# Kernel optimization log

Hardware: AMD Instinct MI355X
Metric: run time of the kernel (lower is better)

## Reference

```python
import jax, jax.numpy as jnp
import numpy as np

EPS = 1e-5
DEG = 2  # polynomial degree of each resgconv layer (adj powers 0..DEG-1)


def _bn(x):
    # repo's functional batchnorm(x, axis=1): standardize over the node axis per event
    m = x.mean(axis=1, keepdims=True)
    s = x.std(axis=1, keepdims=True)
    return (x - m) / (s + EPS)


def _adj(phi, eta):
    # Gaussian kernel of squared euclidean distance in the (eta, phi) plane
    d2 = (phi[:, :, None] - phi[:, None, :]) ** 2 + (eta[:, :, None] - eta[:, None, :]) ** 2
    return jnp.exp(-d2)  # [B, N, N]


def _resgconv(adj, x, W, b, Wr, br):
    # x: [B, C_in, N]; spread = concat of adj^k @ x for k in 0..DEG-1 over channels
    sp = [x]
    cur = x
    for _ in range(DEG - 1):
        cur = jnp.einsum('bij,bcj->bci', adj, cur)
        sp.append(cur)
    sp = jnp.concatenate(sp, axis=1)  # [B, C_in*DEG, N]
    out = jnp.einsum('oc,bcn->bon', W, sp) + b[None, :, None]
    res = jnp.einsum('oc,bcn->bon', Wr, x) + br[None, :, None]  # residual shortcut
    return jax.nn.relu(out) + res


def setup_inputs():
    key = jax.random.key(0)
    ks = jax.random.split(key, 32)
    B, N = 16, 2048
    dims = [3, 64, 64, 64, 64]
    inp = {
        'e': jax.random.normal(ks[0], (B, N), dtype=jnp.float32),
        'phi': jax.random.normal(ks[1], (B, N), dtype=jnp.float32),
        'eta': jax.random.normal(ks[2], (B, N), dtype=jnp.float32),
    }
    for i in range(4):
        cin, cout = dims[i], dims[i + 1]
        inp[f'W{i}'] = jax.random.normal(ks[3 + 4 * i], (cout, cin * DEG)) * (1.0 / np.sqrt(cin * DEG))
        inp[f'b{i}'] = jnp.zeros((cout,), dtype=jnp.float32)
        inp[f'Wr{i}'] = jax.random.normal(ks[4 + 4 * i], (cout, cin)) * (1.0 / np.sqrt(cin))
        inp[f'br{i}'] = jnp.zeros((cout,), dtype=jnp.float32)
    inp['fcW'] = jax.random.normal(ks[30], (1, dims[-1])) * (1.0 / np.sqrt(dims[-1]))
    inp['fcb'] = jnp.zeros((1,), dtype=jnp.float32)
    return inp


def reference(e, phi, eta, W0, b0, Wr0, br0, W1, b1, Wr1, br1, W2, b2, Wr2, br2, W3, b3, Wr3, br3, fcW, fcb):
    en = _bn(e)
    adj = _adj(phi, eta)
    x = jnp.stack([en, _bn(eta), _bn(phi)], axis=1)  # [B, 3, N]
    for (W, b, Wr, br) in ((W0, b0, Wr0, br0), (W1, b1, Wr1, br1), (W2, b2, Wr2, br2), (W3, b3, Wr3, br3)):
        x = _resgconv(adj, x, W, b, Wr, br)
    pooled = x.mean(axis=2)  # [B, C]
    out = pooled @ fcW.T + fcb  # [B, 1]
    return out[:, 0]
```

## Files before the change

### kernel.cpp

```cpp
#include <hip/hip_runtime.h>
#include <hip/hip_bf16.h>

#define NN 2048
#define NB 16
#define XT_PITCH 88
#define CAT_PITCH 136
#define RED_PITCH 132

typedef __attribute__((ext_vector_type(8))) short short8;
typedef __attribute__((ext_vector_type(4))) float f32x4;

static __device__ __forceinline__ float bfbits2f(short s) {
  unsigned int u = ((unsigned int)(unsigned short)s) << 16;
  float f; __builtin_memcpy(&f, &u, 4); return f;
}
static __device__ __forceinline__ short f2bfbits(float f) {
  __hip_bfloat16 h = __float2bfloat16(f);
  unsigned short us; __builtin_memcpy(&us, &h, 2); return (short)us;
}
static __device__ __forceinline__ float exp2_fast(float x) {
#if __has_builtin(__builtin_amdgcn_exp2f)
  return __builtin_amdgcn_exp2f(x);
#else
  return exp2f(x);
#endif
}
static __device__ __forceinline__ unsigned pack2bf(float f0, float f1) {
  unsigned u0, u1;
  __builtin_memcpy(&u0, &f0, 4);
  __builtin_memcpy(&u1, &f1, 4);
  return __builtin_amdgcn_perm(u1 + 0x8000u, u0 + 0x8000u, 0x07060302u);
}

__global__ __launch_bounds__(256) void bn_kernel(
    const float* __restrict__ e, const float* __restrict__ phi,
    const float* __restrict__ eta, __hip_bfloat16* __restrict__ x0) {
  const int b = blockIdx.x;
  const int c = blockIdx.y;
  const int t = threadIdx.x;
  __hip_bfloat16* out = x0 + ((size_t)b * 64 + c) * NN;
  if (c >= 3) {
    short8 z = {0, 0, 0, 0, 0, 0, 0, 0};
    for (int idx = t * 8; idx < NN; idx += 256 * 8) *(short8*)&out[idx] = z;
    return;
  }
  const float* src = (c == 0 ? e : (c == 1 ? eta : phi)) + (size_t)b * NN;
  float sum = 0.f, sq = 0.f;
  for (int idx = t * 4; idx < NN; idx += 256 * 4) {
    float4 v = *(const float4*)&src[idx];
    sum += v.x + v.y + v.z + v.w;
    sq += v.x * v.x + v.y * v.y + v.z * v.z + v.w * v.w;
  }
  __shared__ float rs[256], rq[256];
  rs[t] = sum; rq[t] = sq;
  __syncthreads();
  for (int off = 128; off > 0; off >>= 1) {
    if (t < off) { rs[t] += rs[t + off]; rq[t] += rq[t + off]; }
    __syncthreads();
  }
  const float m = rs[0] * (1.f / NN);
  const float var = fmaxf(rq[0] * (1.f / NN) - m * m, 0.f);
  const float rinv = 1.f / (sqrtf(var) + 1e-5f);
  for (int idx = t * 4; idx < NN; idx += 256 * 4) {
    float4 v = *(const float4*)&src[idx];
    out[idx + 0] = __float2bfloat16((v.x - m) * rinv);
    out[idx + 1] = __float2bfloat16((v.y - m) * rinv);
    out[idx + 2] = __float2bfloat16((v.z - m) * rinv);
    out[idx + 3] = __float2bfloat16((v.w - m) * rinv);
  }
}

__global__ __launch_bounds__(256) void prep_kernel(
    const float* __restrict__ W0, const float* __restrict__ W1,
    const float* __restrict__ W2, const float* __restrict__ W3,
    const float* __restrict__ R0, const float* __restrict__ R1,
    const float* __restrict__ R2, const float* __restrict__ R3,
    short* __restrict__ blob) {
  const int layer = blockIdx.x;
  const float* W = layer == 0 ? W0 : layer == 1 ? W1 : layer == 2 ? W2 : W3;
  const float* R = layer == 0 ? R0 : layer == 1 ? R1 : layer == 2 ? R2 : R3;
  const int CIN = layer == 0 ? 3 : 64;
  short* base = blob + layer * 24576;
  for (int f = threadIdx.x; f < 8192; f += 256) {
    int e = f & 7, lane = (f >> 3) & 63, ks = (f >> 9) & 3, os = f >> 11;
    int o = os * 16 + (lane & 15);
    int k = ks * 32 + (lane >> 4) * 8 + e;
    float v = 0.f;
    if (k < 64) { if (k < CIN) v = W[o * 2 * CIN + k]; }
    else { int c = k - 64; if (c < CIN) v = W[o * 2 * CIN + CIN + c]; }
    short hi = f2bfbits(v);
    base[f] = hi;
    base[8192 + f] = f2bfbits(v - bfbits2f(hi));
  }
  for (int f = threadIdx.x; f < 4096; f += 256) {
    int e = f & 7, lane = (f >> 3) & 63, ks = (f >> 9) & 1, os = f >> 10;
    int o = os * 16 + (lane & 15);
    int k = ks * 32 + (lane >> 4) * 8 + e;
    float v = (k < CIN) ? R[o * CIN + k] : 0.f;
    short hi = f2bfbits(v);
    base[16384 + f] = hi;
    base[20480 + f] = f2bfbits(v - bfbits2f(hi));
  }
}

__global__ __launch_bounds__(512, 2) void layer_kernel(
    const float* __restrict__ phi, const float* __restrict__ eta,
    const __hip_bfloat16* __restrict__ x, const short* __restrict__ wcat,
    const short* __restrict__ wrb, const float* __restrict__ bias,
    const float* __restrict__ brs, __hip_bfloat16* __restrict__ xo) {
  const int b = blockIdx.y;
  const int i0 = blockIdx.x * 128;
  const int tid = threadIdx.x;
  const int wave = tid >> 6;
  const int lane = tid & 63;
  const int c0 = lane & 15;
  const int hh = lane >> 4;
  const int koff = hh * 8;
  const int qw = wave & 3;
  const int h = wave >> 2;
  const int tl = tid & 255;

  __shared__ __align__(16) char smem[62464];
  float* phs = (float*)smem;
  float* ehs = (float*)(smem + 8192);
  short* out_t = (short*)smem;
  short* xt_base = (short*)(smem + 17408);
  float* red = (float*)(smem + 17408);
  short* cat = (short*)(smem + 17408);

  const float SC = 1.20112240872f;
  {
    const float* pb = phi + (size_t)b * NN;
    const float* eb = eta + (size_t)b * NN;
    for (int idx = tid; idx < NN; idx += 512) {
      phs[idx] = pb[idx] * SC;
      ehs[idx] = eb[idx] * SC;
    }
  }
  const short* xb = (const short*)(x + (size_t)b * 64 * NN);
  {
    const int c = tl >> 2, q = tl & 3;
    const short* g = xb + (size_t)c * NN + h * 1024 + q * 16;
    short8 s0 = *(const short8*)g;
    short8 s1 = *(const short8*)(g + 8);
    short* d = xt_base + (h * 2 + 0) * (64 * XT_PITCH) + c * XT_PITCH + q * 16;
    *(short8*)d = s0;
    *(short8*)(d + 8) = s1;
  }
  __syncthreads();

  const float pi0 = phs[i0 + qw * 32 + c0];
  const float ei0 = ehs[i0 + qw * 32 + c0];
  const float pi1 = phs[i0 + qw * 32 + 16 + c0];
  const float ei1 = ehs[i0 + qw * 32 + 16 + c0];

  f32x4 acc0[4], acc1[4];
#pragma unroll
  for (int cs = 0; cs < 4; ++cs) {
    acc0[cs] = (f32x4){0.f, 0.f, 0.f, 0.f};
    acc1[cs] = (f32x4){0.f, 0.f, 0.f, 0.f};
  }

#pragma unroll 1
  for (int t = 0; t < 16; ++t) {
    short8 ng0, ng1;
    short* nd = nullptr;
    if (t < 15) {
      const int c = tl >> 2, q = tl & 3;
      const short* g = xb + (size_t)c * NN + h * 1024 + (t + 1) * 64 + q * 16;
      ng0 = *(const short8*)g;
      ng1 = *(const short8*)(g + 8);
      nd = xt_base + (h * 2 + ((t + 1) & 1)) * (64 * XT_PITCH) + c * XT_PITCH + q * 16;
    }
    const short* xcur = xt_base + (h * 2 + (t & 1)) * (64 * XT_PITCH);
#pragma unroll
    for (int kk = 0; kk < 2; ++kk) {
      const int jb = h * 1024 + t * 64 + kk * 32 + koff;
      float pj[8], ej[8];
      *(float4*)&pj[0] = *(const float4*)&phs[jb];
      *(float4*)&pj[4] = *(const float4*)&phs[jb + 4];
      *(float4*)&ej[0] = *(const float4*)&ehs[jb];
      *(float4*)&ej[4] = *(const float4*)&ehs[jb + 4];
      unsigned au0[4], au1[4];
#pragma unroll
      for (int p = 0; p < 4; ++p) {
        float dpa = pi0 - pj[2 * p],     dea = ei0 - ej[2 * p];
        float dpb = pi0 - pj[2 * p + 1], deb = ei0 - ej[2 * p + 1];
        float fa = exp2_fast(-(dpa * dpa + dea * dea));
        float fb = exp2_fast(-(dpb * dpb + deb * deb));
        au0[p] = pack2bf(fa, fb);
        float dpc = pi1 - pj[2 * p],     dec = ei1 - ej[2 * p];
        float dpd = pi1 - pj[2 * p + 1], ded = ei1 - ej[2 * p + 1];
        float fc = exp2_fast(-(dpc * dpc + dec * dec));
        float fd = exp2_fast(-(dpd * dpd + ded * ded));
        au1[p] = pack2bf(fc, fd);
      }
      short8 af0, af1;
      __builtin_memcpy(&af0, au0, 16);
      __builtin_memcpy(&af1, au1, 16);
      const short* xk = xcur + kk * 32 + koff;
#pragma unroll
      for (int cs = 0; cs < 4; ++cs) {
        short8 bf = *(const short8*)&xk[(cs * 16 + c0) * XT_PITCH];
        acc0[cs] = __builtin_amdgcn_mfma_f32_16x16x32_bf16(af0, bf, acc0[cs], 0, 0, 0);
        acc1[cs] = __builtin_amdgcn_mfma_f32_16x16x32_bf16(af1, bf, acc1[cs], 0, 0, 0);
      }
    }
    if (t < 15) {
      *(short8*)nd = ng0;
      *(short8*)(nd + 8) = ng1;
    }
    __syncthreads();
  }

  if (h == 1) {
#pragma unroll
    for (int cs = 0; cs < 4; ++cs) {
      const int c = cs * 16 + c0;
      *(f32x4*)&red[c * RED_PITCH + qw * 32 + hh * 4] = acc0[cs];
      *(f32x4*)&red[c * RED_PITCH + qw * 32 + 16 + hh * 4] = acc1[cs];
    }
  }
  __syncthreads();
  if (h == 0) {
#pragma unroll
    for (int cs = 0; cs < 4; ++cs) {
      const int c = cs * 16 + c0;
      f32x4 r0 = *(const f32x4*)&red[c * RED_PITCH + qw * 32 + hh * 4];
      f32x4 r1 = *(const f32x4*)&red[c * RED_PITCH + qw * 32 + 16 + hh * 4];
      acc0[cs] += r0;
      acc1[cs] += r1;
    }
  }
  __syncthreads();

  if (h == 0) {
#pragma unroll
    for (int cs = 0; cs < 4; ++cs)
#pragma unroll
      for (int r = 0; r < 4; ++r) {
        const int row0 = qw * 32 + hh * 4 + r;
        cat[row0 * CAT_PITCH + 64 + cs * 16 + c0] = f2bfbits(acc0[cs][r]);
        cat[(row0 + 16) * CAT_PITCH + 64 + cs * 16 + c0] = f2bfbits(acc1[cs][r]);
      }
  }
  {
    const int c = tid >> 3, part = tid & 7;
    const short* xr = xb + (size_t)c * NN + i0 + part * 16;
    short8 v0 = *(const short8*)xr;
    short8 v1 = *(const short8*)(xr + 8);
#pragma unroll
    for (int q = 0; q < 8; ++q) cat[(part * 16 + q) * CAT_PITCH + c] = v0[q];
#pragma unroll
    for (int q = 0; q < 8; ++q) cat[(part * 16 + 8 + q) * CAT_PITCH + c] = v1[q];
  }
  __syncthreads();

  {
    const int irl = wave * 16 + c0;
    short8 bf[4];
#pragma unroll
    for (int ks = 0; ks < 4; ++ks)
      bf[ks] = *(const short8*)&cat[irl * CAT_PITCH + ks * 32 + koff];
#pragma unroll
    for (int os = 0; os < 4; ++os) {
      f32x4 a1 = (f32x4){0.f, 0.f, 0.f, 0.f};
      f32x4 a2 = (f32x4){0.f, 0.f, 0.f, 0.f};
#pragma unroll
      for (int ks = 0; ks < 4; ++ks) {
        short8 whi = *(const short8*)&wcat[(size_t)(((os * 4 + ks) * 64) + lane) * 8];
        short8 wlo = *(const short8*)&wcat[8192 + (size_t)(((os * 4 + ks) * 64) + lane) * 8];
        a1 = __builtin_amdgcn_mfma_f32_16x16x32_bf16(whi, bf[ks], a1, 0, 0, 0);
        a1 = __builtin_amdgcn_mfma_f32_16x16x32_bf16(wlo, bf[ks], a1, 0, 0, 0);
      }
#pragma unroll
      for (int ks = 0; ks < 2; ++ks) {
        short8 rhi = *(const short8*)&wrb[(size_t)(((os * 2 + ks) * 64) + lane) * 8];
        short8 rlo = *(const short8*)&wrb[4096 + (size_t)(((os * 2 + ks) * 64) + lane) * 8];
        a2 = __builtin_amdgcn_mfma_f32_16x16x32_bf16(rhi, bf[ks], a2, 0, 0, 0);
        a2 = __builtin_amdgcn_mfma_f32_16x16x32_bf16(rlo, bf[ks], a2, 0, 0, 0);
      }
#pragma unroll
      for (int r = 0; r < 4; ++r) {
        const int o = os * 16 + hh * 4 + r;
        float v = fmaxf(a1[r] + bias[o], 0.f) + a2[r] + brs[o];
        out_t[o * CAT_PITCH + wave * 16 + c0] = f2bfbits(v);
      }
    }
  }
  __syncthreads();

  {
    const int o = tid >> 3, part = tid & 7;
    short8 v0 = *(const short8*)&out_t[o * CAT_PITCH + part * 16];
    short8 v1 = *(const short8*)&out_t[o * CAT_PITCH + part * 16 + 8];
    short* dst = (short*)xo + (size_t)b * 64 * NN + (size_t)o * NN + i0 + part * 16;
    *(short8*)dst = v0;
    *(short8*)(dst + 8) = v1;
  }
}

__global__ __launch_bounds__(256) void final_kernel(
    const __hip_bfloat16* __restrict__ x, const float* __restrict__ fcW,
    const float* __restrict__ fcb, float* __restrict__ out) {
  const int b = blockIdx.x;
  const short* xb = (const short*)(x + (size_t)b * 64 * NN);
  float acc = 0.f;
  for (int f = threadIdx.x * 8; f < 64 * NN; f += 256 * 8) {
    short8 v = *(const short8*)&xb[f];
    const float w = fcW[f >> 11];
    float ss = 0.f;
#pragma unroll
    for (int e8 = 0; e8 < 8; ++e8) ss += bfbits2f(v[e8]);
    acc += w * ss;
  }
  __shared__ float red[256];
  red[threadIdx.x] = acc;
  __syncthreads();
  for (int off = 128; off > 0; off >>= 1) {
    if ((int)threadIdx.x < off) red[threadIdx.x] += red[threadIdx.x + off];
    __syncthreads();
  }
  if (threadIdx.x == 0) out[b] = red[0] * (1.f / NN) + fcb[0];
}

extern "C" void kernel_launch(void* const* d_in, const int* in_sizes, int n_in,
                              void* d_out, int out_size, void* d_ws, size_t ws_size,
                              hipStream_t stream) {
  const float* e   = (const float*)d_in[0];
  const float* phi = (const float*)d_in[1];
  const float* eta = (const float*)d_in[2];
  const float* W[4]  = {(const float*)d_in[3],  (const float*)d_in[7],
                        (const float*)d_in[11], (const float*)d_in[15]};
  const float* bb[4] = {(const float*)d_in[4],  (const float*)d_in[8],
                        (const float*)d_in[12], (const float*)d_in[16]};
  const float* Wr[4] = {(const float*)d_in[5],  (const float*)d_in[9],
                        (const float*)d_in[13], (const float*)d_in[17]};
  const float* br[4] = {(const float*)d_in[6],  (const float*)d_in[10],
                        (const float*)d_in[14], (const float*)d_in[18]};
  const float* fcW = (const float*)d_in[19];
  const float* fcb = (const float*)d_in[20];
  float* outp = (float*)d_out;

  const size_t XSZ = (size_t)NB * 64 * NN;
  __hip_bfloat16* xA = (__hip_bfloat16*)d_ws;
  __hip_bfloat16* xB = xA + XSZ;
  short* blob = (short*)(xB + XSZ);

  dim3 bn_grid(NB, 64);
  bn_kernel<<<bn_grid, 256, 0, stream>>>(e, phi, eta, xA);
  prep_kernel<<<4, 256, 0, stream>>>(W[0], W[1], W[2], W[3],
                                     Wr[0], Wr[1], Wr[2], Wr[3], blob);

  dim3 lgrid(NN / 128, NB);
  const __hip_bfloat16* xin = xA;
  __hip_bfloat16* xout = xB;
  for (int l = 0; l < 4; ++l) {
    const short* lb = blob + l * 24576;
    layer_kernel<<<lgrid, 512, 0, stream>>>(phi, eta, xin, lb, lb + 16384,
                                            bb[l], br[l], xout);
    const __hip_bfloat16* t = xout; xout = (__hip_bfloat16*)xin; xin = t;
  }
  final_kernel<<<NB, 256, 0, stream>>>(xA, fcW, fcb, outp);
}
```

Baseline: 249.4 us.

## Split j-range across 8 waves with 4x4 MFMA tiles, async global-to-LDS staging

The layer kernel moves to 1024-thread blocks. The j (neighbour) range is split into 8 groups, and each wave computes a 64x64 tile of adjacency-times-x with 4 row tiles, so each loaded x fragment feeds four MFMAs. The x chunks are staged into a swizzled LDS layout with global_load_lds instead of register round trips. Partial sums are reduced across wave groups through LDS in a two-stage tree. The change uses 144KB of shared memory and many more accumulator registers, which may limit occupancy, and the launch bound of (1024,4) is unlikely to be achievable.

```diff
diff --git a/kernel.cpp b/kernel.cpp
--- a/kernel.cpp
+++ b/kernel.cpp
@@ -3,9 +3,10 @@
 
 #define NN 2048
 #define NB 16
-#define XT_PITCH 88
 #define CAT_PITCH 136
-#define RED_PITCH 132
+#define RSLOT_PITCH 68
+#define XT_OFF 16384
+#define SMEM_BYTES 147456
 
 typedef __attribute__((ext_vector_type(8))) short short8;
 typedef __attribute__((ext_vector_type(4))) float f32x4;
@@ -30,6 +31,12 @@
   __builtin_memcpy(&u0, &f0, 4);
   __builtin_memcpy(&u1, &f1, 4);
   return __builtin_amdgcn_perm(u1 + 0x8000u, u0 + 0x8000u, 0x07060302u);
+}
+
+static __device__ __forceinline__ void gload_lds16(const void* g, void* l) {
+  __builtin_amdgcn_global_load_lds(
+      (const __attribute__((address_space(1))) unsigned int*)g,
+      (__attribute__((address_space(3))) unsigned int*)l, 16, 0, 0);
 }
 
 __global__ __launch_bounds__(256) void bn_kernel(
@@ -103,7 +110,23 @@
   }
 }
 
-__global__ __launch_bounds__(512, 2) void layer_kernel(
+static __device__ __forceinline__ void stage_chunk(
+    const short* __restrict__ xb, char* smem, int wave, int lane, int tt) {
+  const int par = tt & 1;
+#pragma unroll
+  for (int q = 0; q < 4; ++q) {
+    const int s = wave * 4 + q;
+    const int jgs = s >> 3;
+    const int sl = s & 7;
+    const int ch = sl * 8 + (lane >> 3);
+    const int jc8 = (lane & 7) ^ (ch & 7);
+    const short* g = xb + (size_t)ch * NN + jgs * 256 + tt * 64 + jc8 * 8;
+    char* l = smem + XT_OFF + jgs * 16384 + par * 8192 + sl * 1024;
+    gload_lds16(g, l);
+  }
+}
+
+__global__ __launch_bounds__(1024, 4) void layer_kernel(
     const float* __restrict__ phi, const float* __restrict__ eta,
     const __hip_bfloat16* __restrict__ x, const short* __restrict__ wcat,
     const short* __restrict__ wrb, const float* __restrict__ bias,
@@ -116,187 +139,186 @@
   const int c0 = lane & 15;
   const int hh = lane >> 4;
   const int koff = hh * 8;
-  const int qw = wave & 3;
-  const int h = wave >> 2;
-  const int tl = tid & 255;
-
-  __shared__ __align__(16) char smem[62464];
+  const int rh = wave & 1;
+  const int jg = wave >> 1;
+
+  __shared__ __align__(16) char smem[SMEM_BYTES];
   float* phs = (float*)smem;
-  float* ehs = (float*)(smem + 8192);
-  short* out_t = (short*)smem;
-  short* xt_base = (short*)(smem + 17408);
-  float* red = (float*)(smem + 17408);
-  short* cat = (short*)(smem + 17408);
+  float* ehs = phs + NN;
 
   const float SC = 1.20112240872f;
   {
     const float* pb = phi + (size_t)b * NN;
     const float* eb = eta + (size_t)b * NN;
-    for (int idx = tid; idx < NN; idx += 512) {
+    for (int idx = tid; idx < NN; idx += 1024) {
       phs[idx] = pb[idx] * SC;
       ehs[idx] = eb[idx] * SC;
     }
   }
   const short* xb = (const short*)(x + (size_t)b * 64 * NN);
-  {
-    const int c = tl >> 2, q = tl & 3;
-    const short* g = xb + (size_t)c * NN + h * 1024 + q * 16;
-    short8 s0 = *(const short8*)g;
-    short8 s1 = *(const short8*)(g + 8);
-    short* d = xt_base + (h * 2 + 0) * (64 * XT_PITCH) + c * XT_PITCH + q * 16;
-    *(short8*)d = s0;
-    *(short8*)(d + 8) = s1;
-  }
-  __syncthreads();
-
-  const float pi0 = phs[i0 + qw * 32 + c0];
-  const float ei0 = ehs[i0 + qw * 32 + c0];
-  const float pi1 = phs[i0 + qw * 32 + 16 + c0];
-  const float ei1 = ehs[i0 + qw * 32 + 16 + c0];
-
-  f32x4 acc0[4], acc1[4];
-#pragma unroll
-  for (int cs = 0; cs < 4; ++cs) {
-    acc0[cs] = (f32x4){0.f, 0.f, 0.f, 0.f};
-    acc1[cs] = (f32x4){0.f, 0.f, 0.f, 0.f};
-  }
-
-#pragma unroll 1
-  for (int t = 0; t < 16; ++t) {
-    short8 ng0, ng1;
-    short* nd = nullptr;
-    if (t < 15) {
-      const int c = tl >> 2, q = tl & 3;
-      const short* g = xb + (size_t)c * NN + h * 1024 + (t + 1) * 64 + q * 16;
-      ng0 = *(const short8*)g;
-      ng1 = *(const short8*)(g + 8);
-      nd = xt_base + (h * 2 + ((t + 1) & 1)) * (64 * XT_PITCH) + c * XT_PITCH + q * 16;
-    }
-    const short* xcur = xt_base + (h * 2 + (t & 1)) * (64 * XT_PITCH);
+  stage_chunk(xb, smem, wave, lane, 0);
+  __syncthreads();
+
+  float pi_[4], ei_[4];
+#pragma unroll
+  for (int mt = 0; mt < 4; ++mt) {
+    const int row = i0 + rh * 64 + mt * 16 + c0;
+    pi_[mt] = phs[row];
+    ei_[mt] = ehs[row];
+  }
+
+  f32x4 acc[4][4];
+#pragma unroll
+  for (int mt = 0; mt < 4; ++mt)
+#pragma unroll
+    for (int cs = 0; cs < 4; ++cs) acc[mt][cs] = (f32x4){0.f, 0.f, 0.f, 0.f};
+
+  for (int t = 0; t < 4; ++t) {
+    if (t < 3) stage_chunk(xb, smem, wave, lane, t + 1);
+    const char* xbuf = smem + XT_OFF + jg * 16384 + (t & 1) * 8192;
+    const int jbase = jg * 256 + t * 64;
 #pragma unroll
     for (int kk = 0; kk < 2; ++kk) {
-      const int jb = h * 1024 + t * 64 + kk * 32 + koff;
+      const int jb = jbase + kk * 32 + koff;
       float pj[8], ej[8];
       *(float4*)&pj[0] = *(const float4*)&phs[jb];
       *(float4*)&pj[4] = *(const float4*)&phs[jb + 4];
       *(float4*)&ej[0] = *(const float4*)&ehs[jb];
       *(float4*)&ej[4] = *(const float4*)&ehs[jb + 4];
-      unsigned au0[4], au1[4];
-#pragma unroll
-      for (int p = 0; p < 4; ++p) {
-        float dpa = pi0 - pj[2 * p],     dea = ei0 - ej[2 * p];
-        float dpb = pi0 - pj[2 * p + 1], deb = ei0 - ej[2 * p + 1];
-        float fa = exp2_fast(-(dpa * dpa + dea * dea));
-        float fb = exp2_fast(-(dpb * dpb + deb * deb));
-        au0[p] = pack2bf(fa, fb);
-        float dpc = pi1 - pj[2 * p],     dec = ei1 - ej[2 * p];
-        float dpd = pi1 - pj[2 * p + 1], ded = ei1 - ej[2 * p + 1];
-        float fc = exp2_fast(-(dpc * dpc + dec * dec));
-        float fd = exp2_fast(-(dpd * dpd + ded * ded));
-        au1[p] = pack2bf(fc, fd);
-      }
-      short8 af0, af1;
-      __builtin_memcpy(&af0, au0, 16);
-      __builtin_memcpy(&af1, au1, 16);
-      const short* xk = xcur + kk * 32 + koff;
+      short8 af[4];
+#pragma unroll
+      for (int mt = 0; mt < 4; ++mt) {
+        unsigned au[4];
+#pragma unroll
+        for (int p = 0; p < 4; ++p) {
+          float dpa = pi_[mt] - pj[2 * p],     dea = ei_[mt] - ej[2 * p];
+          float dpb = pi_[mt] - pj[2 * p + 1], deb = ei_[mt] - ej[2 * p + 1];
+          float fa = exp2_fast(-(dpa * dpa + dea * dea));
+          float fb = exp2_fast(-(dpb * dpb + deb * deb));
+          au[p] = pack2bf(fa, fb);
+        }
+        __builtin_memcpy(&af[mt], au, 16);
+      }
+      const int jc = kk * 32 + koff;
 #pragma unroll
       for (int cs = 0; cs < 4; ++cs) {
-        short8 bf = *(const short8*)&xk[(cs * 16 + c0) * XT_PITCH];
-        acc0[cs] = __builtin_amdgcn_mfma_f32_16x16x32_bf16(af0, bf, acc0[cs], 0, 0, 0);
-        acc1[cs] = __builtin_amdgcn_mfma_f32_16x16x32_bf16(af1, bf, acc1[cs], 0, 0, 0);
-      }
-    }
-    if (t < 15) {
-      *(short8*)nd = ng0;
-      *(short8*)(nd + 8) = ng1;
+        const int ch = cs * 16 + c0;
+        const int boff = (ch * 128 + jc * 2) ^ ((ch & 7) << 4);
+        short8 bf = *(const short8*)(xbuf + boff);
+#pragma unroll
+        for (int mt = 0; mt < 4; ++mt)
+          acc[mt][cs] = __builtin_amdgcn_mfma_f32_16x16x32_bf16(af[mt], bf,
+                                                               acc[mt][cs], 0, 0, 0);
+      }
     }
     __syncthreads();
   }
 
-  if (h == 1) {
-#pragma unroll
-    for (int cs = 0; cs < 4; ++cs) {
-      const int c = cs * 16 + c0;
-      *(f32x4*)&red[c * RED_PITCH + qw * 32 + hh * 4] = acc0[cs];
-      *(f32x4*)&red[c * RED_PITCH + qw * 32 + 16 + hh * 4] = acc1[cs];
+  float* red = (float*)smem;
+  const int slot_sz = 64 * RSLOT_PITCH;
+  if (jg >= 4) {
+    float* sp = red + ((jg - 4) * 2 + rh) * slot_sz;
+#pragma unroll
+    for (int mt = 0; mt < 4; ++mt)
+#pragma unroll
+      for (int cs = 0; cs < 4; ++cs)
+        *(f32x4*)&sp[(cs * 16 + c0) * RSLOT_PITCH + mt * 16 + hh * 4] = acc[mt][cs];
+  }
+  __syncthreads();
+  if (jg < 4) {
+    const float* sp = red + (jg * 2 + rh) * slot_sz;
+#pragma unroll
+    for (int mt = 0; mt < 4; ++mt)
+#pragma unroll
+      for (int cs = 0; cs < 4; ++cs)
+        acc[mt][cs] += *(const f32x4*)&sp[(cs * 16 + c0) * RSLOT_PITCH + mt * 16 + hh * 4];
+  }
+  __syncthreads();
+  if (jg >= 1 && jg < 4) {
+    float* sp = red + ((jg - 1) * 2 + rh) * slot_sz;
+#pragma unroll
+    for (int mt = 0; mt < 4; ++mt)
+#pragma unroll
+      for (int cs = 0; cs < 4; ++cs)
+        *(f32x4*)&sp[(cs * 16 + c0) * RSLOT_PITCH + mt * 16 + hh * 4] = acc[mt][cs];
+  }
+  __syncthreads();
+  if (jg == 0) {
+#pragma unroll
+    for (int k = 0; k < 3; ++k) {
+      const float* sp = red + (k * 2 + rh) * slot_sz;
+#pragma unroll
+      for (int mt = 0; mt < 4; ++mt)
+#pragma unroll
+        for (int cs = 0; cs < 4; ++cs)
+          acc[mt][cs] += *(const f32x4*)&sp[(cs * 16 + c0) * RSLOT_PITCH + mt * 16 + hh * 4];
     }
   }
   __syncthreads();
-  if (h == 0) {
-#pragma unroll
-    for (int cs = 0; cs < 4; ++cs) {
-      const int c = cs * 16 + c0;
-      f32x4 r0 = *(const f32x4*)&red[c * RED_PITCH + qw * 32 + hh * 4];
-      f32x4 r1 = *(const f32x4*)&red[c * RED_PITCH + qw * 32 + 16 + hh * 4];
-      acc0[cs] += r0;
-      acc1[cs] += r1;
-    }
-  }
-  __syncthreads();
-
-  if (h == 0) {
-#pragma unroll
-    for (int cs = 0; cs < 4; ++cs)
-#pragma unroll
-      for (int r = 0; r < 4; ++r) {
-        const int row0 = qw * 32 + hh * 4 + r;
-        cat[row0 * CAT_PITCH + 64 + cs * 16 + c0] = f2bfbits(acc0[cs][r]);
-        cat[(row0 + 16) * CAT_PITCH + 64 + cs * 16 + c0] = f2bfbits(acc1[cs][r]);
-      }
+
+  short* cat = (short*)smem;
+  short* out_t = (short*)(smem + 128 * CAT_PITCH * 2);
+  if (jg == 0) {
+#pragma unroll
+    for (int mt = 0; mt < 4; ++mt)
+#pragma unroll
+      for (int cs = 0; cs < 4; ++cs)
+#pragma unroll
+        for (int r = 0; r < 4; ++r) {
+          const int irow = rh * 64 + mt * 16 + hh * 4 + r;
+          cat[irow * CAT_PITCH + 64 + cs * 16 + c0] = f2bfbits(acc[mt][cs][r]);
+        }
   }
   {
-    const int c = tid >> 3, part = tid & 7;
-    const short* xr = xb + (size_t)c * NN + i0 + part * 16;
-    short8 v0 = *(const short8*)xr;
-    short8 v1 = *(const short8*)(xr + 8);
-#pragma unroll
-    for (int q = 0; q < 8; ++q) cat[(part * 16 + q) * CAT_PITCH + c] = v0[q];
-#pragma unroll
-    for (int q = 0; q < 8; ++q) cat[(part * 16 + 8 + q) * CAT_PITCH + c] = v1[q];
+    const int c = tid & 63, rp = tid >> 6;
+    short8 v = *(const short8*)&xb[(size_t)c * NN + i0 + rp * 8];
+#pragma unroll
+    for (int q = 0; q < 8; ++q) cat[(rp * 8 + q) * CAT_PITCH + c] = v[q];
   }
   __syncthreads();
 
   {
-    const int irl = wave * 16 + c0;
-    short8 bf[4];
+    const int it = wave & 7;
+    const int oh = wave >> 3;
+    const int irl = it * 16 + c0;
+    short8 bfx[4];
 #pragma unroll
     for (int ks = 0; ks < 4; ++ks)
-      bf[ks] = *(const short8*)&cat[irl * CAT_PITCH + ks * 32 + koff];
-#pragma unroll
-    for (int os = 0; os < 4; ++os) {
+      bfx[ks] = *(const short8*)&cat[irl * CAT_PITCH + ks * 32 + koff];
+#pragma unroll
+    for (int osl = 0; osl < 2; ++osl) {
+      const int os = oh * 2 + osl;
       f32x4 a1 = (f32x4){0.f, 0.f, 0.f, 0.f};
       f32x4 a2 = (f32x4){0.f, 0.f, 0.f, 0.f};
 #pragma unroll
       for (int ks = 0; ks < 4; ++ks) {
         short8 whi = *(const short8*)&wcat[(size_t)(((os * 4 + ks) * 64) + lane) * 8];
         short8 wlo = *(const short8*)&wcat[8192 + (size_t)(((os * 4 + ks) * 64) + lane) * 8];
-        a1 = __builtin_amdgcn_mfma_f32_16x16x32_bf16(whi, bf[ks], a1, 0, 0, 0);
-        a1 = __builtin_amdgcn_mfma_f32_16x16x32_bf16(wlo, bf[ks], a1, 0, 0, 0);
+        a1 = __builtin_amdgcn_mfma_f32_16x16x32_bf16(whi, bfx[ks], a1, 0, 0, 0);
+        a1 = __builtin_amdgcn_mfma_f32_16x16x32_bf16(wlo, bfx[ks], a1, 0, 0, 0);
       }
 #pragma unroll
       for (int ks = 0; ks < 2; ++ks) {
         short8 rhi = *(const short8*)&wrb[(size_t)(((os * 2 + ks) * 64) + lane) * 8];
         short8 rlo = *(const short8*)&wrb[4096 + (size_t)(((os * 2 + ks) * 64) + lane) * 8];
-        a2 = __builtin_amdgcn_mfma_f32_16x16x32_bf16(rhi, bf[ks], a2, 0, 0, 0);
-        a2 = __builtin_amdgcn_mfma_f32_16x16x32_bf16(rlo, bf[ks], a2, 0, 0, 0);
+        a2 = __builtin_amdgcn_mfma_f32_16x16x32_bf16(rhi, bfx[ks], a2, 0, 0, 0);
+        a2 = __builtin_amdgcn_mfma_f32_16x16x32_bf16(rlo, bfx[ks], a2, 0, 0, 0);
       }
 #pragma unroll
       for (int r = 0; r < 4; ++r) {
         const int o = os * 16 + hh * 4 + r;
         float v = fmaxf(a1[r] + bias[o], 0.f) + a2[r] + brs[o];
-        out_t[o * CAT_PITCH + wave * 16 + c0] = f2bfbits(v);
+        out_t[o * CAT_PITCH + it * 16 + c0] = f2bfbits(v);
       }
     }
   }
   __syncthreads();
 
   {
-    const int o = tid >> 3, part = tid & 7;
-    short8 v0 = *(const short8*)&out_t[o * CAT_PITCH + part * 16];
-    short8 v1 = *(const short8*)&out_t[o * CAT_PITCH + part * 16 + 8];
-    short* dst = (short*)xo + (size_t)b * 64 * NN + (size_t)o * NN + i0 + part * 16;
-    *(short8*)dst = v0;
-    *(short8*)(dst + 8) = v1;
+    const int o = tid >> 4, part = tid & 15;
+    short8 v = *(const short8*)&out_t[o * CAT_PITCH + part * 8];
+    short* dst = (short*)xo + (size_t)b * 64 * NN + (size_t)o * NN + i0 + part * 8;
+    *(short8*)dst = v;
   }
 }
 
@@ -357,8 +379,8 @@
   __hip_bfloat16* xout = xB;
   for (int l = 0; l < 4; ++l) {
     const short* lb = blob + l * 24576;
-    layer_kernel<<<lgrid, 512, 0, stream>>>(phi, eta, xin, lb, lb + 16384,
-                                            bb[l], br[l], xout);
+    layer_kernel<<<lgrid, 1024, 0, stream>>>(phi, eta, xin, lb, lb + 16384,
+                                             bb[l], br[l], xout);
     const __hip_bfloat16* t = xout; xout = (__hip_bfloat16*)xin; xin = t;
   }
   final_kernel<<<NB, 256, 0, stream>>>(xA, fcW, fcb, outp);
```

New measurement: 247.3 us. About the same (-0.9%).
